# Optimization experiments

Hardware: AMD Instinct MI355X
Metric: run time of the kernel (lower is better)

The kernel has to match this reference:

```python
import jax, jax.numpy as jnp
import numpy as np

BATCH, SEQ, INPUT_SIZE, RESERVOIR = 32, 2048, 256, 512


def setup_inputs() -> dict:
    key = jax.random.key(0)
    k_x, k_w, k_d = jax.random.split(key, 3)
    x = jax.random.normal(k_x, (BATCH, SEQ, INPUT_SIZE), dtype=jnp.float32)
    # input_projection weight: uniform(-1, 1), shape [R, input_size]
    W_in = jax.random.uniform(k_w, (RESERVOIR, INPUT_SIZE), dtype=jnp.float32, minval=-1.0, maxval=1.0)
    # diagonal of state_projection: uniform(-0.5, 0.5)
    d = jax.random.uniform(k_d, (RESERVOIR,), dtype=jnp.float32, minval=-0.5, maxval=0.5)
    return {"x": x, "W_in": W_in, "d": d}


def reference(x, W_in, d):
    B, T, _ = x.shape
    R = d.shape[0]
    # input projection: [B, T, R]
    u = jnp.einsum('bti,ri->btr', x, W_in)

    # recurrence: state_t = tanh(d * state_{t-1} + u_t)  (leak gate is dead code: 0*old + 1*new)
    # torch loop fills indices 1..T-1 of all_states (T+1 slots), then returns [:, 1:],
    # so the final returned timestep is all zeros.
    def step(state, u_t):
        new_state = jnp.tanh(d * state + u_t)
        return new_state, new_state

    init = jnp.zeros((B, R), dtype=x.dtype)
    u_tm = jnp.swapaxes(u[:, 1:, :], 0, 1)  # time-major [T-1, B, R]
    _, states = jax.lax.scan(step, init, u_tm)
    states = jnp.swapaxes(states, 0, 1)  # [B, T-1, R]
    tail = jnp.zeros((B, 1, R), dtype=x.dtype)
    return jnp.concatenate([states, tail], axis=1)  # [B, T, R]
```

## Files before the change

### kernel.cpp

```cpp
#include <hip/hip_runtime.h>

#define BATCH 32
#define SEQT  2048
#define INSZ  256
#define RSV   512
#define MTOT  (BATCH * SEQT)
#define BM 128
#define BN 128
#define BK 32
#define LSA 40
#define PADM 65600

#define K2LOG2E 2.8853900817779268f

using f16x8 = __attribute__((ext_vector_type(8))) _Float16;
using f16x4 = __attribute__((ext_vector_type(4))) _Float16;
using f32x4 = __attribute__((ext_vector_type(4))) float;

typedef __attribute__((address_space(1))) unsigned int as1_u32;
typedef __attribute__((address_space(3))) unsigned int as3_u32;
#define GLDS16(gp, lp) __builtin_amdgcn_global_load_lds((as1_u32*)(gp), (as3_u32*)(lp), 16, 0, 0)

static __device__ __forceinline__ float esn_step(float s, float u, float dK) {
    float z  = __builtin_fmaf(dK, s, u * K2LOG2E);
    float e  = __builtin_amdgcn_exp2f(z);
    float rc = __builtin_amdgcn_rcpf(1.0f + e);
    return __builtin_fmaf(-2.0f, rc, 1.0f);
}


__global__ __launch_bounds__(256) void esn_convw(const float* __restrict__ W,
                                                 _Float16* __restrict__ W16) {
    const int i = blockIdx.x * 256 + threadIdx.x;
    float4 v = *(const float4*)(W + (size_t)i * 4);
    float w4[4] = {v.x, v.y, v.z, v.w};
    f16x4 h, l;
    #pragma unroll
    for (int j = 0; j < 4; ++j) {
        _Float16 hh = (_Float16)w4[j];
        h[j] = hh;
        l[j] = (_Float16)(w4[j] - (float)hh);
    }
    *(f16x4*)(W16 + (size_t)i * 4) = h;
    *(f16x4*)(W16 + (size_t)RSV * INSZ + (size_t)i * 4) = l;
}

__global__ __launch_bounds__(256) void esn_gemm_f(const float* __restrict__ X,
                                                  const _Float16* __restrict__ W16,
                                                  _Float16* __restrict__ U16T) {
    __shared__ _Float16 Ash[BM * LSA];
    __shared__ _Float16 Bh[BM * BK];
    __shared__ _Float16 Bl[BM * BK];

    const int tid  = threadIdx.x;
    const int lane = tid & 63;
    const int wid  = tid >> 6;
    const int wr   = wid >> 1, wc = wid & 1;
    const int lgc = (blockIdx.x & 7) * 256 + (blockIdx.x >> 3);
    const int bm = lgc >> 2, bn = lgc & 3;

    const int srow = tid >> 3;
    const int scol = (tid & 7) * 4;

    f32x4 acc[4][4] = {};

    for (int ks = 0; ks < INSZ / BK; ++ks) {
        __syncthreads();
        #pragma unroll
        for (int q = 0; q < 2; ++q) {
            const int c   = (wid * 2 + q) * 64 + lane;
            const int row = c >> 2, col = (c & 3) * 8;
            const _Float16* gh = W16 + (size_t)(bn * BM + row) * INSZ + ks * BK + col;
            GLDS16(gh, &Bh[(wid * 2 + q) * 512]);
            GLDS16(gh + (size_t)RSV * INSZ, &Bl[(wid * 2 + q) * 512]);
        }
        #pragma unroll
        for (int p = 0; p < 4; ++p) {
            const int row = srow + p * 32;
            float4 av = *(const float4*)(X + (size_t)(bm * BM + row) * INSZ + ks * BK + scol);
            float a4[4] = {av.x, av.y, av.z, av.w};
            f16x4 ah;
            #pragma unroll
            for (int j = 0; j < 4; ++j) ah[j] = (_Float16)a4[j];
            *(f16x4*)&Ash[row * LSA + scol] = ah;
        }
        __syncthreads();

        f16x8 af[4], bfh[4], bfl[4];
        #pragma unroll
        for (int m = 0; m < 4; ++m)
            af[m] = *(const f16x8*)&Ash[(wr * 64 + m * 16 + (lane & 15)) * LSA + (lane >> 4) * 8];
        #pragma unroll
        for (int n = 0; n < 4; ++n) {
            const int rr = (wc * 64 + n * 16 + (lane & 15)) * BK + (lane >> 4) * 8;
            bfh[n] = *(const f16x8*)&Bh[rr];
            bfl[n] = *(const f16x8*)&Bl[rr];
        }
        #pragma unroll
        for (int m = 0; m < 4; ++m)
            #pragma unroll
            for (int n = 0; n < 4; ++n) {
                acc[m][n] = __builtin_amdgcn_mfma_f32_16x16x32_f16(af[m], bfh[n], acc[m][n], 0, 0, 0);
                acc[m][n] = __builtin_amdgcn_mfma_f32_16x16x32_f16(af[m], bfl[n], acc[m][n], 0, 0, 0);
            }
    }

    #pragma unroll
    for (int m = 0; m < 4; ++m) {
        const int row0 = bm * BM + wr * 64 + m * 16 + (lane >> 4) * 4;
        #pragma unroll
        for (int n = 0; n < 4; ++n) {
            const int col = bn * BN + wc * 64 + n * 16 + (lane & 15);
            f32x4 v = acc[m][n];
            f16x4 o;
            #pragma unroll
            for (int j = 0; j < 4; ++j) o[j] = (_Float16)v[j];
            *(f16x4*)(U16T + (size_t)col * PADM + row0) = o;
        }
    }
}

__global__ __launch_bounds__(256) void esn_recur_f(const _Float16* __restrict__ U16T,
                                                   const float* __restrict__ D,
                                                   float* __restrict__ OUT) {
    const int tid  = threadIdx.x;
    const int half = blockIdx.x & 1;
    const int pair = blockIdx.x >> 1;
    const int b    = pair >> 3, seg = pair & 7;
    const int r    = half * 256 + tid;

    const _Float16* urow = U16T + (size_t)r * PADM + b * SEQT;
    float* obase = OUT + (size_t)b * SEQT * RSV + r;
    const float dK = D[r] * K2LOG2E;
    const int t0 = seg * 256;

    float s = 0.0f;
    if (seg) {
        #pragma unroll
        for (int k = 0; k < 32; ++k)
            s = esn_step(s, (float)urow[t0 - 31 + k], dK);
    }

    _Float16 bufA[8], bufB[8];
    #pragma unroll
    for (int j = 0; j < 8; ++j) bufA[j] = urow[t0 + 1 + j];
    #pragma unroll
    for (int j = 0; j < 8; ++j) bufB[j] = urow[t0 + 9 + j];

#define PROC8F(buf, tt) do {                                  \
    _Pragma("unroll")                                         \
    for (int j = 0; j < 8; ++j) {                             \
        s = esn_step(s, (float)buf[j], dK);                   \
        obase[(size_t)((tt) + j) * RSV] = s;                  \
        int idx = (tt) + j + 17;                              \
        idx = idx < SEQT ? idx : SEQT - 1;                    \
        buf[j] = urow[idx];                                   \
    }                                                         \
} while (0)

    int t = t0;
    for (int it = 0; it < 16; ++it) {
        PROC8F(bufA, t);
        PROC8F(bufB, t + 8);
        t += 16;
    }
#undef PROC8F
    if (seg == 7) obase[(size_t)(SEQT - 1) * RSV] = 0.0f;
}


__global__ __launch_bounds__(256) void esn_gemm_fb(const float* __restrict__ X,
                                                   const float* __restrict__ W,
                                                   float* __restrict__ U) {
    __shared__ _Float16 Ash[BM * LSA];
    __shared__ _Float16 Bsh[BN * 72];

    const int tid  = threadIdx.x;
    const int lane = tid & 63;
    const int wid  = tid >> 6;
    const int wr   = wid >> 1, wc = wid & 1;
    const int bm   = blockIdx.x >> 2, bn = blockIdx.x & 3;
    const int srow = tid >> 3;
    const int scol = (tid & 7) * 4;

    f32x4 acc[4][4] = {};

    for (int ks = 0; ks < INSZ / BK; ++ks) {
        __syncthreads();
        #pragma unroll
        for (int p = 0; p < 4; ++p) {
            const int row = srow + p * 32;
            float4 av = *(const float4*)(X + (size_t)(bm * BM + row) * INSZ + ks * BK + scol);
            float4 bv = *(const float4*)(W + (size_t)(bn * BN + row) * INSZ + ks * BK + scol);
            float a4[4] = {av.x, av.y, av.z, av.w};
            float b4[4] = {bv.x, bv.y, bv.z, bv.w};
            f16x4 ah, bh, bl;
            #pragma unroll
            for (int j = 0; j < 4; ++j) {
                ah[j] = (_Float16)a4[j];
                _Float16 h = (_Float16)b4[j];
                bh[j] = h;
                bl[j] = (_Float16)(b4[j] - (float)h);
            }
            *(f16x4*)&Ash[row * LSA + scol] = ah;
            *(f16x4*)&Bsh[row * 72 + scol] = bh;
            *(f16x4*)&Bsh[row * 72 + 32 + scol] = bl;
        }
        __syncthreads();

        f16x8 af[4], bfh[4], bfl[4];
        #pragma unroll
        for (int m = 0; m < 4; ++m)
            af[m] = *(const f16x8*)&Ash[(wr * 64 + m * 16 + (lane & 15)) * LSA + (lane >> 4) * 8];
        #pragma unroll
        for (int n = 0; n < 4; ++n) {
            const _Float16* p = &Bsh[(wc * 64 + n * 16 + (lane & 15)) * 72 + (lane >> 4) * 8];
            bfh[n] = *(const f16x8*)p;
            bfl[n] = *(const f16x8*)(p + 32);
        }
        #pragma unroll
        for (int m = 0; m < 4; ++m)
            #pragma unroll
            for (int n = 0; n < 4; ++n) {
                acc[m][n] = __builtin_amdgcn_mfma_f32_16x16x32_f16(af[m], bfh[n], acc[m][n], 0, 0, 0);
                acc[m][n] = __builtin_amdgcn_mfma_f32_16x16x32_f16(af[m], bfl[n], acc[m][n], 0, 0, 0);
            }
    }

    #pragma unroll
    for (int m = 0; m < 4; ++m) {
        const int row = bm * BM + wr * 64 + m * 16 + (lane >> 4) * 4;
        #pragma unroll
        for (int n = 0; n < 4; ++n) {
            const int col = bn * BN + wc * 64 + n * 16 + (lane & 15);
            f32x4 v = acc[m][n];
            #pragma unroll
            for (int j = 0; j < 4; ++j)
                U[(size_t)(row + j) * RSV + col] = v[j];
        }
    }
}

__global__ __launch_bounds__(64) void esn_recur_fb(float* __restrict__ OUT,
                                                   const float* __restrict__ D) {
    const int gid = blockIdx.x * 64 + threadIdx.x;
    const int b = gid >> 9;
    const int r = gid & (RSV - 1);
    float* base = OUT + (size_t)b * SEQT * RSV + r;
    const float dK = D[r] * K2LOG2E;
    float s = 0.0f;

    float bA[8], bB[8], bC[8], bD[8];
    #pragma unroll
    for (int j = 0; j < 8; ++j) bA[j] = base[(size_t)(1 + j) * RSV];
    #pragma unroll
    for (int j = 0; j < 8; ++j) bB[j] = base[(size_t)(9 + j) * RSV];
    #pragma unroll
    for (int j = 0; j < 8; ++j) bC[j] = base[(size_t)(17 + j) * RSV];
    #pragma unroll
    for (int j = 0; j < 8; ++j) bD[j] = base[(size_t)(25 + j) * RSV];

#define PROC8B(buf, tt) do {                                  \
    _Pragma("unroll")                                         \
    for (int j = 0; j < 8; ++j) {                             \
        s = esn_step(s, buf[j], dK);                          \
        base[(size_t)((tt) + j) * RSV] = s;                   \
        int idx = (tt) + 33 + j;                              \
        idx = idx < SEQT ? idx : SEQT - 1;                    \
        buf[j] = base[(size_t)idx * RSV];                     \
    }                                                         \
} while (0)

    int t = 0;
    for (int it = 0; it < 63; ++it) {
        PROC8B(bA, t);
        PROC8B(bB, t + 8);
        PROC8B(bC, t + 16);
        PROC8B(bD, t + 24);
        t += 32;
    }
#undef PROC8B
    #pragma unroll
    for (int j = 0; j < 8; ++j) { s = esn_step(s, bA[j], dK); base[(size_t)(2016 + j) * RSV] = s; }
    #pragma unroll
    for (int j = 0; j < 8; ++j) { s = esn_step(s, bB[j], dK); base[(size_t)(2024 + j) * RSV] = s; }
    #pragma unroll
    for (int j = 0; j < 8; ++j) { s = esn_step(s, bC[j], dK); base[(size_t)(2032 + j) * RSV] = s; }
    #pragma unroll
    for (int j = 0; j < 7; ++j) { s = esn_step(s, bD[j], dK); base[(size_t)(2040 + j) * RSV] = s; }

    base[(size_t)(SEQT - 1) * RSV] = 0.0f;
}

extern "C" void kernel_launch(void* const* d_in, const int* in_sizes, int n_in,
                              void* d_out, int out_size, void* d_ws, size_t ws_size,
                              hipStream_t stream) {
    const float* X = (const float*)d_in[0];
    const float* W = (const float*)d_in[1];
    const float* D = (const float*)d_in[2];
    float* OUT = (float*)d_out;

    const size_t W16_BYTES  = (size_t)2 * RSV * INSZ * sizeof(_Float16);
    const size_t U16T_BYTES = (size_t)RSV * PADM * sizeof(_Float16);
    if (ws_size >= W16_BYTES + U16T_BYTES) {
        _Float16* W16  = (_Float16*)d_ws;
        _Float16* U16T = (_Float16*)((char*)d_ws + W16_BYTES);
        esn_convw<<<dim3(RSV * INSZ / 4 / 256), dim3(256), 0, stream>>>(W, W16);
        esn_gemm_f<<<dim3((MTOT / BM) * (RSV / BN)), dim3(256), 0, stream>>>(X, W16, U16T);
        esn_recur_f<<<dim3(BATCH * 8 * 2), dim3(256), 0, stream>>>(U16T, D, OUT);
    } else {
        esn_gemm_fb<<<dim3((MTOT / BM) * (RSV / BN)), dim3(256), 0, stream>>>(X, W, OUT);
        esn_recur_fb<<<dim3(BATCH * RSV / 64), dim3(64), 0, stream>>>(OUT, D);
    }
}
```

Baseline: 299.1 us.

## Store U row-major, pre-tile W16 for LDS, and reorganize A shared layout

The intermediate projection U is now stored row-major [B*T, R] in fp16 instead of transposed per-reservoir rows. The recurrence kernel therefore reads coalesced across threads (consecutive r) at each timestep rather than strided per-thread rows. W is pre-tiled into the exact LDS tile layout so global_load_lds copies are contiguous, and the A tile in shared memory is split into k-quarter planes to change bank access patterns. The tradeoff is that GEMM epilogue stores become scalar 2-byte writes strided by row, which may be less efficient than the previous 8-byte column stores.

```diff
diff --git a/kernel.cpp b/kernel.cpp
--- a/kernel.cpp
+++ b/kernel.cpp
@@ -9,7 +9,8 @@
 #define BN 128
 #define BK 32
 #define LSA 40
-#define PADM 65600
+#define ASTR 1040
+#define LOPLANE 131072
 
 #define K2LOG2E 2.8853900817779268f
 
@@ -30,27 +31,31 @@
 
 
 __global__ __launch_bounds__(256) void esn_convw(const float* __restrict__ W,
-                                                 _Float16* __restrict__ W16) {
+                                                 _Float16* __restrict__ W16T) {
     const int i = blockIdx.x * 256 + threadIdx.x;
-    float4 v = *(const float4*)(W + (size_t)i * 4);
-    float w4[4] = {v.x, v.y, v.z, v.w};
-    f16x4 h, l;
-    #pragma unroll
-    for (int j = 0; j < 4; ++j) {
-        _Float16 hh = (_Float16)w4[j];
+    const int bn = i >> 12, ks = (i >> 9) & 7, c = i & 511;
+    const int q = c >> 7, row = c & 127;
+    const float* src = W + (size_t)(bn * 128 + row) * INSZ + ks * 32 + q * 8;
+    float4 v0 = *(const float4*)src;
+    float4 v1 = *(const float4*)(src + 4);
+    float w8[8] = {v0.x, v0.y, v0.z, v0.w, v1.x, v1.y, v1.z, v1.w};
+    f16x8 h, l;
+    #pragma unroll
+    for (int j = 0; j < 8; ++j) {
+        _Float16 hh = (_Float16)w8[j];
         h[j] = hh;
-        l[j] = (_Float16)(w4[j] - (float)hh);
-    }
-    *(f16x4*)(W16 + (size_t)i * 4) = h;
-    *(f16x4*)(W16 + (size_t)RSV * INSZ + (size_t)i * 4) = l;
+        l[j] = (_Float16)(w8[j] - (float)hh);
+    }
+    *(f16x8*)(W16T + (size_t)i * 8) = h;
+    *(f16x8*)(W16T + LOPLANE + (size_t)i * 8) = l;
 }
 
 __global__ __launch_bounds__(256) void esn_gemm_f(const float* __restrict__ X,
-                                                  const _Float16* __restrict__ W16,
-                                                  _Float16* __restrict__ U16T) {
-    __shared__ _Float16 Ash[BM * LSA];
-    __shared__ _Float16 Bh[BM * BK];
-    __shared__ _Float16 Bl[BM * BK];
+                                                  const _Float16* __restrict__ W16T,
+                                                  _Float16* __restrict__ U16) {
+    __shared__ _Float16 Ash[4 * ASTR];
+    __shared__ _Float16 Bh[4096];
+    __shared__ _Float16 Bl[4096];
 
     const int tid  = threadIdx.x;
     const int lane = tid & 63;
@@ -61,18 +66,19 @@
 
     const int srow = tid >> 3;
     const int scol = (tid & 7) * 4;
+    const int qa   = scol >> 3;
+    const int ha   = (scol >> 2) & 1;
 
     f32x4 acc[4][4] = {};
 
     for (int ks = 0; ks < INSZ / BK; ++ks) {
         __syncthreads();
         #pragma unroll
-        for (int q = 0; q < 2; ++q) {
-            const int c   = (wid * 2 + q) * 64 + lane;
-            const int row = c >> 2, col = (c & 3) * 8;
-            const _Float16* gh = W16 + (size_t)(bn * BM + row) * INSZ + ks * BK + col;
-            GLDS16(gh, &Bh[(wid * 2 + q) * 512]);
-            GLDS16(gh + (size_t)RSV * INSZ, &Bl[(wid * 2 + q) * 512]);
+        for (int j = 0; j < 2; ++j) {
+            const int cbase = (wid * 2 + j) * 64;
+            const _Float16* gh = W16T + ((size_t)(bn * 8 + ks) * 512 + cbase + lane) * 8;
+            GLDS16(gh, &Bh[cbase * 8]);
+            GLDS16(gh + LOPLANE, &Bl[cbase * 8]);
         }
         #pragma unroll
         for (int p = 0; p < 4; ++p) {
@@ -82,17 +88,18 @@
             f16x4 ah;
             #pragma unroll
             for (int j = 0; j < 4; ++j) ah[j] = (_Float16)a4[j];
-            *(f16x4*)&Ash[row * LSA + scol] = ah;
+            *(f16x4*)&Ash[qa * ASTR + row * 8 + ha * 4] = ah;
         }
         __syncthreads();
 
         f16x8 af[4], bfh[4], bfl[4];
+        const int qf = lane >> 4;
         #pragma unroll
         for (int m = 0; m < 4; ++m)
-            af[m] = *(const f16x8*)&Ash[(wr * 64 + m * 16 + (lane & 15)) * LSA + (lane >> 4) * 8];
+            af[m] = *(const f16x8*)&Ash[qf * ASTR + (wr * 64 + m * 16 + (lane & 15)) * 8];
         #pragma unroll
         for (int n = 0; n < 4; ++n) {
-            const int rr = (wc * 64 + n * 16 + (lane & 15)) * BK + (lane >> 4) * 8;
+            const int rr = qf * 1024 + (wc * 64 + n * 16 + (lane & 15)) * 8;
             bfh[n] = *(const f16x8*)&Bh[rr];
             bfl[n] = *(const f16x8*)&Bl[rr];
         }
@@ -112,49 +119,48 @@
         for (int n = 0; n < 4; ++n) {
             const int col = bn * BN + wc * 64 + n * 16 + (lane & 15);
             f32x4 v = acc[m][n];
-            f16x4 o;
-            #pragma unroll
-            for (int j = 0; j < 4; ++j) o[j] = (_Float16)v[j];
-            *(f16x4*)(U16T + (size_t)col * PADM + row0) = o;
-        }
-    }
-}
-
-__global__ __launch_bounds__(256) void esn_recur_f(const _Float16* __restrict__ U16T,
+            #pragma unroll
+            for (int j = 0; j < 4; ++j)
+                U16[(size_t)(row0 + j) * RSV + col] = (_Float16)v[j];
+        }
+    }
+}
+
+__global__ __launch_bounds__(256) void esn_recur_f(const _Float16* __restrict__ U16,
                                                    const float* __restrict__ D,
                                                    float* __restrict__ OUT) {
     const int tid  = threadIdx.x;
+    const int b    = blockIdx.x >> 4;
+    const int seg  = (blockIdx.x >> 1) & 7;
     const int half = blockIdx.x & 1;
-    const int pair = blockIdx.x >> 1;
-    const int b    = pair >> 3, seg = pair & 7;
     const int r    = half * 256 + tid;
 
-    const _Float16* urow = U16T + (size_t)r * PADM + b * SEQT;
-    float* obase = OUT + (size_t)b * SEQT * RSV + r;
+    const _Float16* ub = U16 + (size_t)b * SEQT * RSV + r;
+    float* ob = OUT + (size_t)b * SEQT * RSV + r;
     const float dK = D[r] * K2LOG2E;
     const int t0 = seg * 256;
 
     float s = 0.0f;
     if (seg) {
-        #pragma unroll
+        #pragma unroll 8
         for (int k = 0; k < 32; ++k)
-            s = esn_step(s, (float)urow[t0 - 31 + k], dK);
+            s = esn_step(s, (float)ub[(size_t)(t0 - 31 + k) * RSV], dK);
     }
 
     _Float16 bufA[8], bufB[8];
     #pragma unroll
-    for (int j = 0; j < 8; ++j) bufA[j] = urow[t0 + 1 + j];
-    #pragma unroll
-    for (int j = 0; j < 8; ++j) bufB[j] = urow[t0 + 9 + j];
+    for (int j = 0; j < 8; ++j) bufA[j] = ub[(size_t)(t0 + 1 + j) * RSV];
+    #pragma unroll
+    for (int j = 0; j < 8; ++j) bufB[j] = ub[(size_t)(t0 + 9 + j) * RSV];
 
 #define PROC8F(buf, tt) do {                                  \
     _Pragma("unroll")                                         \
     for (int j = 0; j < 8; ++j) {                             \
         s = esn_step(s, (float)buf[j], dK);                   \
-        obase[(size_t)((tt) + j) * RSV] = s;                  \
+        ob[(size_t)((tt) + j) * RSV] = s;                     \
         int idx = (tt) + j + 17;                              \
         idx = idx < SEQT ? idx : SEQT - 1;                    \
-        buf[j] = urow[idx];                                   \
+        buf[j] = ub[(size_t)idx * RSV];                       \
     }                                                         \
 } while (0)
 
@@ -165,7 +171,7 @@
         t += 16;
     }
 #undef PROC8F
-    if (seg == 7) obase[(size_t)(SEQT - 1) * RSV] = 0.0f;
+    if (seg == 7) ob[(size_t)(SEQT - 1) * RSV] = 0.0f;
 }
 
 
@@ -300,14 +306,14 @@
     const float* D = (const float*)d_in[2];
     float* OUT = (float*)d_out;
 
-    const size_t W16_BYTES  = (size_t)2 * RSV * INSZ * sizeof(_Float16);
-    const size_t U16T_BYTES = (size_t)RSV * PADM * sizeof(_Float16);
-    if (ws_size >= W16_BYTES + U16T_BYTES) {
-        _Float16* W16  = (_Float16*)d_ws;
-        _Float16* U16T = (_Float16*)((char*)d_ws + W16_BYTES);
-        esn_convw<<<dim3(RSV * INSZ / 4 / 256), dim3(256), 0, stream>>>(W, W16);
-        esn_gemm_f<<<dim3((MTOT / BM) * (RSV / BN)), dim3(256), 0, stream>>>(X, W16, U16T);
-        esn_recur_f<<<dim3(BATCH * 8 * 2), dim3(256), 0, stream>>>(U16T, D, OUT);
+    const size_t W16T_BYTES = (size_t)2 * RSV * INSZ * sizeof(_Float16);
+    const size_t U16_BYTES  = (size_t)MTOT * RSV * sizeof(_Float16);
+    if (ws_size >= W16T_BYTES + U16_BYTES) {
+        _Float16* W16T = (_Float16*)d_ws;
+        _Float16* U16  = (_Float16*)((char*)d_ws + W16T_BYTES);
+        esn_convw<<<dim3(64), dim3(256), 0, stream>>>(W, W16T);
+        esn_gemm_f<<<dim3((MTOT / BM) * (RSV / BN)), dim3(256), 0, stream>>>(X, W16T, U16);
+        esn_recur_f<<<dim3(BATCH * 8 * 2), dim3(256), 0, stream>>>(U16, D, OUT);
     } else {
         esn_gemm_fb<<<dim3((MTOT / BM) * (RSV / BN)), dim3(256), 0, stream>>>(X, W, OUT);
         esn_recur_fb<<<dim3(BATCH * RSV / 64), dim3(64), 0, stream>>>(OUT, D);
```

After: 245.6 us. -17.9%, faster.
